# Optimization experiments

Hardware: AMD Instinct MI355X
Metric: run time of the kernel (lower is better)

Reference implementation:

```python
import jax, jax.numpy as jnp
import numpy as np

B, A = 4096, 8          # episodes, agents per episode
N = B * A               # total nodes
E = B * A * (A - 1)     # fully-connected directed edges within each group
F_IN, D, H, M, NA = 64, 64, 4, 64, 10  # in_feat, gnn_dim, heads, mem_dim, n_actions
NEG_SLOPE = 0.2
LN_EPS = 1e-5


def _build_edge_index():
    base = np.arange(A)
    s = np.repeat(base, A)
    d = np.tile(base, A)
    keep = s != d
    s, d = s[keep], d[keep]                       # [A*(A-1)]
    offs = (np.arange(B) * A)[:, None]
    src = (offs + s[None, :]).reshape(-1)
    dst = (offs + d[None, :]).reshape(-1)
    return jnp.asarray(np.stack([src, dst]), dtype=jnp.int32)  # [2, E]


def setup_inputs() -> dict:
    key = jax.random.key(0)
    ks = jax.random.split(key, 16)
    sc = 0.05
    return {
        "x": jax.random.normal(ks[0], (N, F_IN), jnp.float32),
        "edge_attr": jax.random.normal(ks[1], (E, 3), jnp.float32),
        "hidden": jax.random.normal(ks[2], (N, M), jnp.float32) * sc,
        "edge_index": _build_edge_index(),
        # GATv2 params
        "Wl": jax.random.normal(ks[3], (H * D, F_IN), jnp.float32) * sc,
        "bl": jnp.zeros((H * D,), jnp.float32),
        "Wr": jax.random.normal(ks[4], (H * D, F_IN), jnp.float32) * sc,
        "br": jnp.zeros((H * D,), jnp.float32),
        "We": jax.random.normal(ks[5], (H * D, 3), jnp.float32) * sc,
        "be": jnp.zeros((H * D,), jnp.float32),
        "att": jax.random.normal(ks[6], (H, D), jnp.float32) * sc,
        "bias_g": jnp.zeros((D,), jnp.float32),
        # GRUCell params (gate order r,z,n as in torch)
        "W_ih": jax.random.normal(ks[7], (3 * M, D), jnp.float32) * sc,
        "W_hh": jax.random.normal(ks[8], (3 * M, M), jnp.float32) * sc,
        "b_ih": jnp.zeros((3 * M,), jnp.float32),
        "b_hh": jnp.zeros((3 * M,), jnp.float32),
        # LayerNorm + output Linear
        "ln_g": jnp.ones((M,), jnp.float32),
        "ln_b": jnp.zeros((M,), jnp.float32),
        "Wq": jax.random.normal(ks[9], (NA, M), jnp.float32) * sc,
        "bq": jnp.zeros((NA,), jnp.float32),
    }


def reference(x, edge_attr, hidden, edge_index, Wl, bl, Wr, br, We, be, att,
              bias_g, W_ih, W_hh, b_ih, b_hh, ln_g, ln_b, Wq, bq):
    src, dst = edge_index[0], edge_index[1]
    # GATv2Conv (concat=False -> mean over heads), share_weights=False
    xl = (x @ Wl.T + bl).reshape(N, H, D)          # source projection
    xr = (x @ Wr.T + br).reshape(N, H, D)          # target projection
    ee = (edge_attr @ We.T + be).reshape(E, H, D)  # edge embedding
    m = jax.nn.leaky_relu(xl[src] + xr[dst] + ee, NEG_SLOPE)  # [E,H,D]
    logits = jnp.einsum('ehd,hd->eh', m, att)                  # [E,H]
    lmax = jax.ops.segment_max(logits, dst, num_segments=N)    # [N,H]
    ex = jnp.exp(logits - lmax[dst])
    denom = jax.ops.segment_sum(ex, dst, num_segments=N)       # [N,H]
    alpha = ex / denom[dst]                                    # softmax per target
    agg = jax.ops.segment_sum(alpha[:, :, None] * xl[src], dst, num_segments=N)  # [N,H,D]
    h_gnn = jax.nn.relu(agg.mean(axis=1) + bias_g)             # [N,D]
    # GRUCell
    gi = h_gnn @ W_ih.T + b_ih
    gh = hidden @ W_hh.T + b_hh
    ir, iz, inn = jnp.split(gi, 3, axis=-1)
    hr, hz, hn = jnp.split(gh, 3, axis=-1)
    r = jax.nn.sigmoid(ir + hr)
    z = jax.nn.sigmoid(iz + hz)
    n = jnp.tanh(inn + r * hn)
    h = (1.0 - z) * n + z * hidden                              # [N,M]
    # LayerNorm + Linear head
    mu = h.mean(axis=-1, keepdims=True)
    var = ((h - mu) ** 2).mean(axis=-1, keepdims=True)
    hln = (h - mu) / jnp.sqrt(var + LN_EPS) * ln_g + ln_b
    q = hln @ Wq.T + bq                                         # [N,NA]
    return q, h
```

## Files before the change

kernel.cpp:

```cpp
#include <hip/hip_runtime.h>

typedef unsigned short u16;
typedef __attribute__((ext_vector_type(8))) short bf16x8;
typedef __attribute__((ext_vector_type(4))) float f32x4;

#define NAG 8
#define FIN 64
#define MDIM 64
#define NACT 10
#define EPG 56
#define NTOT 32768
#define ABP 72
#define XLS 296
#define XHS 72

#define U_XR 2368
#define U_RZ 0
#define U_IN 1024
#define U_HN 1536
#define U_LN 2048

__device__ __forceinline__ float b2f(u16 u) {
  return __uint_as_float(((unsigned int)u) << 16);
}
__device__ __forceinline__ u16 f2b(float f) {
  unsigned int x = __float_as_uint(f);
  unsigned int r = x + 0x7fffu + ((x >> 16) & 1u);
  return (u16)(r >> 16);
}

__global__ __launch_bounds__(256) void prep_weights(
    const float* __restrict__ Wl, const float* __restrict__ Wr,
    const float* __restrict__ Wih, const float* __restrict__ Whh,
    u16* __restrict__ wsB)
{
  const int idx = blockIdx.x * 256 + threadIdx.x;
  if (idx >= 56 * 2 * 64) return;
  const int L  = idx & 63;
  const int ks = (idx >> 6) & 1;
  const int T  = idx >> 7;
  const float* W; int row0;
  if      (T < 16) { W = Wl;  row0 = T * 16; }
  else if (T < 32) { W = Wr;  row0 = (T - 16) * 16; }
  else if (T < 44) { W = Wih; row0 = (T - 32) * 16; }
  else             { W = Whh; row0 = (T - 44) * 16; }
  const int row = row0 + (L & 15);
  const int k0  = ks * 32 + (L >> 4) * 8;
  u16 v[8];
#pragma unroll
  for (int j = 0; j < 8; j++) v[j] = f2b(W[row * 64 + k0 + j]);
  *(bf16x8*)(wsB + (size_t)idx * 8) = *(bf16x8*)v;
}

__global__ __launch_bounds__(256, 4) void gnn_rnn_kernel(
    const float* __restrict__ x, const float* __restrict__ edge_attr,
    const float* __restrict__ hidden,
    const float* __restrict__ bl, const float* __restrict__ br,
    const float* __restrict__ We, const float* __restrict__ be,
    const float* __restrict__ att, const float* __restrict__ bias_g,
    const float* __restrict__ b_ih, const float* __restrict__ b_hh,
    const float* __restrict__ ln_g, const float* __restrict__ ln_b,
    const float* __restrict__ Wq, const float* __restrict__ bq,
    const u16* __restrict__ wsB,
    float* __restrict__ d_out)
{
  __shared__ __align__(16) char uraw[10368];
  __shared__ __align__(16) u16 s_xb[NAG * ABP];
  __shared__ __align__(16) u16 s_hidb[NAG * ABP];
  __shared__ __align__(16) u16 s_hgb[NAG * ABP];
  __shared__ __align__(16) float s_hid[NAG * MDIM];
  __shared__ float s_ea[EPG * 3];
  __shared__ __align__(16) u16 s_blb[256], s_brb[256];
  __shared__ __align__(16) u16 s_w0b[288], s_w1b[288], s_w2b[288], s_beb[288], s_attb[288];
  __shared__ float s_alpha[EPG][4];
  __shared__ float s_bih[192], s_bhh[192];

  u16*   uXL = (u16*)uraw;
  u16*   uXR = (u16*)uraw + U_XR;
  float* uF  = (float*)uraw;

  const int t = threadIdx.x;
  const int b = blockIdx.x;
  const int L = t & 63;
  const int w = t >> 6;
  const int q = L >> 4;

  {
    const float* xb = x + b * (NAG * FIN);
    const float* hb = hidden + b * (NAG * MDIM);
#pragma unroll
    for (int i = t; i < NAG * FIN; i += 256) {
      const int a = i >> 6, m = i & 63;
      s_xb[a * ABP + m] = f2b(xb[i]);
      const float hv = hb[i];
      s_hid[a * MDIM + m] = hv;
      s_hidb[a * ABP + m] = f2b(hv);
    }
    const float* eb = edge_attr + b * (EPG * 3);
    if (t < EPG * 3) s_ea[t] = eb[t];
    s_blb[t] = f2b(bl[t]);  s_brb[t] = f2b(br[t]);
    {
      const int h = t >> 6, d = t & 63, idx = h * XHS + d;
      s_beb[idx]  = f2b(be[t]);
      s_attb[idx] = f2b(att[t]);
      s_w0b[idx]  = f2b(We[t * 3]);
      s_w1b[idx]  = f2b(We[t * 3 + 1]);
      s_w2b[idx]  = f2b(We[t * 3 + 2]);
    }
    if (t < 192)  { s_bih[t] = b_ih[t]; s_bhh[t] = b_hh[t]; }
  }
  __syncthreads();

  {
    const int arow = L & 7;
    bf16x8 af0 = *(const bf16x8*)&s_xb[arow * ABP + q * 8];
    bf16x8 af1 = *(const bf16x8*)&s_xb[arow * ABP + 32 + q * 8];
    const bf16x8* wsBv = (const bf16x8*)wsB;
#pragma unroll 4
    for (int i = 0; i < 8; i++) {
      const int T = w * 8 + i;
      f32x4 acc = {0.f, 0.f, 0.f, 0.f};
      acc = __builtin_amdgcn_mfma_f32_16x16x32_bf16(af0, wsBv[(T * 2 + 0) * 64 + L], acc, 0, 0, 0);
      acc = __builtin_amdgcn_mfma_f32_16x16x32_bf16(af1, wsBv[(T * 2 + 1) * 64 + L], acc, 0, 0, 0);
      if (q < 2) {
        const int col = L & 15;
        const int Tm = T & 15;
        const int h = Tm >> 2, d = (Tm & 3) * 16 + col;
        const int gc = Tm * 16 + col;
        if (T < 16) {
          const float bias = b2f(s_blb[gc]);
#pragma unroll
          for (int r = 0; r < 4; r++)
            uXL[(q * 4 + r) * XLS + h * XHS + d] = f2b(acc[r] + bias);
        } else {
          const float bias = b2f(s_brb[gc]);
#pragma unroll
          for (int r = 0; r < 4; r++)
            uXR[(q * 4 + r) * XLS + h * XHS + d] = f2b(acc[r] + bias);
        }
      }
    }
  }
  __syncthreads();

  if (t < EPG * 4) {
    const int e = t % 56, h = t / 56;
    const int s = e / 7, k = e % 7;
    const int j = k + (k >= s ? 1 : 0);
    const float ea0 = s_ea[e * 3], ea1 = s_ea[e * 3 + 1], ea2 = s_ea[e * 3 + 2];
    const u16* xlp = uXL + s * XLS + h * XHS;
    const u16* xrp = uXR + j * XLS + h * XHS;
    const u16* w0p = s_w0b + h * XHS;
    const u16* w1p = s_w1b + h * XHS;
    const u16* w2p = s_w2b + h * XHS;
    const u16* bep = s_beb + h * XHS;
    const u16* atp = s_attb + h * XHS;
    float lg = 0.f;
#pragma unroll 2
    for (int kq = 0; kq < 8; kq++) {
      bf16x8 vxl = *(const bf16x8*)(xlp + kq * 8);
      bf16x8 vxr = *(const bf16x8*)(xrp + kq * 8);
      bf16x8 v0  = *(const bf16x8*)(w0p + kq * 8);
      bf16x8 v1  = *(const bf16x8*)(w1p + kq * 8);
      bf16x8 v2  = *(const bf16x8*)(w2p + kq * 8);
      bf16x8 vb  = *(const bf16x8*)(bep + kq * 8);
      bf16x8 va  = *(const bf16x8*)(atp + kq * 8);
#pragma unroll
      for (int c = 0; c < 8; c++) {
        float mv = b2f((u16)vxl[c]) + b2f((u16)vxr[c])
                 + ea0 * b2f((u16)v0[c]) + ea1 * b2f((u16)v1[c])
                 + ea2 * b2f((u16)v2[c]) + b2f((u16)vb[c]);
        mv = mv > 0.f ? mv : 0.2f * mv;
        lg += mv * b2f((u16)va[c]);
      }
    }
    s_alpha[e][h] = lg;
  }
  __syncthreads();

  if (t < 32) {
    const int j = t >> 2, h = t & 3;
    float mx = -1e30f;
#pragma unroll
    for (int s = 0; s < 8; s++) {
      if (s == j) continue;
      int e = s * 7 + (j > s ? j - 1 : j);
      mx = fmaxf(mx, s_alpha[e][h]);
    }
    float sum = 0.f;
#pragma unroll
    for (int s = 0; s < 8; s++) {
      if (s == j) continue;
      int e = s * 7 + (j > s ? j - 1 : j);
      float ex = __expf(s_alpha[e][h] - mx);
      s_alpha[e][h] = ex;
      sum += ex;
    }
    float inv = 1.f / sum;
#pragma unroll
    for (int s = 0; s < 8; s++) {
      if (s == j) continue;
      int e = s * 7 + (j > s ? j - 1 : j);
      s_alpha[e][h] *= inv;
    }
  }
  __syncthreads();

  if (t < 128) {
    const int jj = t >> 4, dq = t & 15;
    float acc[4] = {0.f, 0.f, 0.f, 0.f};
#pragma unroll 2
    for (int h = 0; h < 4; h++) {
#pragma unroll
      for (int s = 0; s < 8; s++) {
        if (s == jj) continue;
        int e = s * 7 + (jj > s ? jj - 1 : jj);
        float al = s_alpha[e][h];
        const u16* xp = uXL + s * XLS + h * XHS + dq * 4;
        ushort4 xv = *(const ushort4*)xp;
        acc[0] += al * b2f(xv.x);
        acc[1] += al * b2f(xv.y);
        acc[2] += al * b2f(xv.z);
        acc[3] += al * b2f(xv.w);
      }
    }
    const f32x4 bg = *(const f32x4*)(bias_g + dq * 4);
    u16 pk[4];
#pragma unroll
    for (int c = 0; c < 4; c++) {
      float v = acc[c] * 0.25f + bg[c];
      pk[c] = f2b(v > 0.f ? v : 0.f);
    }
    *(uint2*)&s_hgb[jj * ABP + dq * 4] = *(uint2*)pk;
  }
  __syncthreads();

  {
    const int arow = L & 7;
    bf16x8 ag0 = *(const bf16x8*)&s_hgb[arow * ABP + q * 8];
    bf16x8 ag1 = *(const bf16x8*)&s_hgb[arow * ABP + 32 + q * 8];
    bf16x8 ah0 = *(const bf16x8*)&s_hidb[arow * ABP + q * 8];
    bf16x8 ah1 = *(const bf16x8*)&s_hidb[arow * ABP + 32 + q * 8];
    const bf16x8* wsBv = (const bf16x8*)wsB;
#pragma unroll
    for (int i = 0; i < 3; i++) {
      const int T6 = w * 3 + i;
      const int Tg = 32 + T6, Th = 44 + T6;
      f32x4 acci = {0.f, 0.f, 0.f, 0.f};
      acci = __builtin_amdgcn_mfma_f32_16x16x32_bf16(ag0, wsBv[(Tg * 2 + 0) * 64 + L], acci, 0, 0, 0);
      acci = __builtin_amdgcn_mfma_f32_16x16x32_bf16(ag1, wsBv[(Tg * 2 + 1) * 64 + L], acci, 0, 0, 0);
      f32x4 acch = {0.f, 0.f, 0.f, 0.f};
      acch = __builtin_amdgcn_mfma_f32_16x16x32_bf16(ah0, wsBv[(Th * 2 + 0) * 64 + L], acch, 0, 0, 0);
      acch = __builtin_amdgcn_mfma_f32_16x16x32_bf16(ah1, wsBv[(Th * 2 + 1) * 64 + L], acch, 0, 0, 0);
      if (q < 2) {
        const int col = L & 15;
        const int gc = T6 * 16 + col;
        if (T6 < 8) {
#pragma unroll
          for (int r = 0; r < 4; r++)
            uF[U_RZ + (q * 4 + r) * 128 + gc] = acci[r] + acch[r] + s_bih[gc] + s_bhh[gc];
        } else {
#pragma unroll
          for (int r = 0; r < 4; r++) {
            uF[U_IN + (q * 4 + r) * 64 + gc - 128] = acci[r] + s_bih[gc];
            uF[U_HN + (q * 4 + r) * 64 + gc - 128] = acch[r] + s_bhh[gc];
          }
        }
      }
    }
  }
  __syncthreads();

  {
    const float lng = ln_g[L];
    const float lnb = ln_b[L];
#pragma unroll
    for (int rr = 0; rr < 2; rr++) {
      const int a = w + rr * 4, m = L;
      float rz_r = uF[U_RZ + a * 128 + m];
      float rz_z = uF[U_RZ + a * 128 + 64 + m];
      float inn  = uF[U_IN + a * 64 + m];
      float hn   = uF[U_HN + a * 64 + m];
      float r = 1.f / (1.f + __expf(-rz_r));
      float z = 1.f / (1.f + __expf(-rz_z));
      float xg = inn + r * hn;
      xg = fminf(fmaxf(xg, -20.f), 20.f);
      float e2 = __expf(2.f * xg);
      float n = (e2 - 1.f) / (e2 + 1.f);
      float hv = (1.f - z) * n + z * s_hid[a * MDIM + m];
      d_out[NTOT * NACT + (b * NAG + a) * MDIM + m] = hv;
      float sum = hv;
#pragma unroll
      for (int off = 1; off < 64; off <<= 1) sum += __shfl_xor(sum, off, 64);
      float mu = sum * (1.f / 64.f);
      float dv = hv - mu;
      float s2 = dv * dv;
#pragma unroll
      for (int off = 1; off < 64; off <<= 1) s2 += __shfl_xor(s2, off, 64);
      float var = s2 * (1.f / 64.f);
      uF[U_LN + a * 68 + m] = dv * rsqrtf(var + 1e-5f) * lng + lnb;
    }
  }
  __syncthreads();

  if (t < NAG * NACT) {
    const int a = t / NACT, o = t % NACT;
    float acc = bq[o];
    const float4* lv = (const float4*)(uF + U_LN + a * 68);
    const float4* wv = (const float4*)(Wq + o * 64);
#pragma unroll 4
    for (int kq = 0; kq < 16; kq++) {
      float4 l4 = lv[kq], w4 = wv[kq];
      acc += l4.x * w4.x + l4.y * w4.y + l4.z * w4.z + l4.w * w4.w;
    }
    d_out[(b * NAG + a) * NACT + o] = acc;
  }
}

extern "C" void kernel_launch(void* const* d_in, const int* in_sizes, int n_in,
                              void* d_out, int out_size, void* d_ws, size_t ws_size,
                              hipStream_t stream) {
  const int N  = in_sizes[0] / FIN;
  const int Bn = N / NAG;
  u16* wsB = (u16*)d_ws;

  prep_weights<<<28, 256, 0, stream>>>(
      (const float*)d_in[4],
      (const float*)d_in[6],
      (const float*)d_in[12],
      (const float*)d_in[13],
      wsB);

  gnn_rnn_kernel<<<Bn, 256, 0, stream>>>(
      (const float*)d_in[0], (const float*)d_in[1], (const float*)d_in[2],
      (const float*)d_in[5],
      (const float*)d_in[7],
      (const float*)d_in[8],
      (const float*)d_in[9],
      (const float*)d_in[10],
      (const float*)d_in[11],
      (const float*)d_in[14],
      (const float*)d_in[15],
      (const float*)d_in[16], (const float*)d_in[17],
      (const float*)d_in[18], (const float*)d_in[19],
      wsB, (float*)d_out);
}
```

Before: 161.4 us.

## Process two episodes per block to fill MFMA rows and halve block count

```diff
diff --git a/kernel.cpp b/kernel.cpp
--- a/kernel.cpp
+++ b/kernel.cpp
@@ -5,6 +5,7 @@
 typedef __attribute__((ext_vector_type(4))) float f32x4;
 
 #define NAG 8
+#define NAGB 16
 #define FIN 64
 #define MDIM 64
 #define NACT 10
@@ -14,11 +15,11 @@
 #define XLS 296
 #define XHS 72
 
-#define U_XR 2368
+#define U_XR 4736
 #define U_RZ 0
-#define U_IN 1024
-#define U_HN 1536
-#define U_LN 2048
+#define U_IN 2048
+#define U_HN 3072
+#define U_LN 4096
 
 __device__ __forceinline__ float b2f(u16 u) {
   return __uint_as_float(((unsigned int)u) << 16);
@@ -64,15 +65,14 @@
     const u16* __restrict__ wsB,
     float* __restrict__ d_out)
 {
-  __shared__ __align__(16) char uraw[10368];
-  __shared__ __align__(16) u16 s_xb[NAG * ABP];
-  __shared__ __align__(16) u16 s_hidb[NAG * ABP];
-  __shared__ __align__(16) u16 s_hgb[NAG * ABP];
-  __shared__ __align__(16) float s_hid[NAG * MDIM];
-  __shared__ float s_ea[EPG * 3];
+  __shared__ __align__(16) char uraw[20736];
+  __shared__ __align__(16) u16 s_xb[NAGB * ABP];
+  __shared__ __align__(16) u16 s_hidb[NAGB * ABP];
+  __shared__ __align__(16) u16 s_hgb[NAGB * ABP];
+  __shared__ float s_ea[2 * EPG * 3];
   __shared__ __align__(16) u16 s_blb[256], s_brb[256];
   __shared__ __align__(16) u16 s_w0b[288], s_w1b[288], s_w2b[288], s_beb[288], s_attb[288];
-  __shared__ float s_alpha[EPG][4];
+  __shared__ float s_alpha[2 * EPG][4];
   __shared__ float s_bih[192], s_bhh[192];
 
   u16*   uXL = (u16*)uraw;
@@ -86,18 +86,16 @@
   const int q = L >> 4;
 
   {
-    const float* xb = x + b * (NAG * FIN);
-    const float* hb = hidden + b * (NAG * MDIM);
-#pragma unroll
-    for (int i = t; i < NAG * FIN; i += 256) {
+    const float* xb = x + b * (NAGB * FIN);
+    const float* hb = hidden + b * (NAGB * MDIM);
+#pragma unroll
+    for (int i = t; i < NAGB * FIN; i += 256) {
       const int a = i >> 6, m = i & 63;
       s_xb[a * ABP + m] = f2b(xb[i]);
-      const float hv = hb[i];
-      s_hid[a * MDIM + m] = hv;
-      s_hidb[a * ABP + m] = f2b(hv);
-    }
-    const float* eb = edge_attr + b * (EPG * 3);
-    if (t < EPG * 3) s_ea[t] = eb[t];
+      s_hidb[a * ABP + m] = f2b(hb[i]);
+    }
+    const float* eb = edge_attr + b * (2 * EPG * 3);
+    for (int i = t; i < 2 * EPG * 3; i += 256) s_ea[i] = eb[i];
     s_blb[t] = f2b(bl[t]);  s_brb[t] = f2b(br[t]);
     {
       const int h = t >> 6, d = t & 63, idx = h * XHS + d;
@@ -112,7 +110,7 @@
   __syncthreads();
 
   {
-    const int arow = L & 7;
+    const int arow = L & 15;
     bf16x8 af0 = *(const bf16x8*)&s_xb[arow * ABP + q * 8];
     bf16x8 af1 = *(const bf16x8*)&s_xb[arow * ABP + 32 + q * 8];
     const bf16x8* wsBv = (const bf16x8*)wsB;
@@ -122,76 +120,78 @@
       f32x4 acc = {0.f, 0.f, 0.f, 0.f};
       acc = __builtin_amdgcn_mfma_f32_16x16x32_bf16(af0, wsBv[(T * 2 + 0) * 64 + L], acc, 0, 0, 0);
       acc = __builtin_amdgcn_mfma_f32_16x16x32_bf16(af1, wsBv[(T * 2 + 1) * 64 + L], acc, 0, 0, 0);
-      if (q < 2) {
-        const int col = L & 15;
-        const int Tm = T & 15;
-        const int h = Tm >> 2, d = (Tm & 3) * 16 + col;
-        const int gc = Tm * 16 + col;
-        if (T < 16) {
-          const float bias = b2f(s_blb[gc]);
-#pragma unroll
-          for (int r = 0; r < 4; r++)
-            uXL[(q * 4 + r) * XLS + h * XHS + d] = f2b(acc[r] + bias);
-        } else {
-          const float bias = b2f(s_brb[gc]);
-#pragma unroll
-          for (int r = 0; r < 4; r++)
-            uXR[(q * 4 + r) * XLS + h * XHS + d] = f2b(acc[r] + bias);
+      const int col = L & 15;
+      const int Tm = T & 15;
+      const int h = Tm >> 2, d = (Tm & 3) * 16 + col;
+      const int gc = Tm * 16 + col;
+      if (T < 16) {
+        const float bias = b2f(s_blb[gc]);
+#pragma unroll
+        for (int r = 0; r < 4; r++)
+          uXL[(q * 4 + r) * XLS + h * XHS + d] = f2b(acc[r] + bias);
+      } else {
+        const float bias = b2f(s_brb[gc]);
+#pragma unroll
+        for (int r = 0; r < 4; r++)
+          uXR[(q * 4 + r) * XLS + h * XHS + d] = f2b(acc[r] + bias);
+      }
+    }
+  }
+  __syncthreads();
+
+  for (int ep = 0; ep < 2; ep++) {
+    if (t < EPG * 4) {
+      const int e = t % 56, h = t / 56;
+      const int s = e / 7, k = e % 7;
+      const int j = k + (k >= s ? 1 : 0);
+      const int eg = ep * EPG + e;
+      const float ea0 = s_ea[eg * 3], ea1 = s_ea[eg * 3 + 1], ea2 = s_ea[eg * 3 + 2];
+      const u16* xlp = uXL + (ep * 8 + s) * XLS + h * XHS;
+      const u16* xrp = uXR + (ep * 8 + j) * XLS + h * XHS;
+      const u16* w0p = s_w0b + h * XHS;
+      const u16* w1p = s_w1b + h * XHS;
+      const u16* w2p = s_w2b + h * XHS;
+      const u16* bep = s_beb + h * XHS;
+      const u16* atp = s_attb + h * XHS;
+      float lg = 0.f;
+#pragma unroll 2
+      for (int kq = 0; kq < 8; kq++) {
+        bf16x8 vxl = *(const bf16x8*)(xlp + kq * 8);
+        bf16x8 vxr = *(const bf16x8*)(xrp + kq * 8);
+        bf16x8 v0  = *(const bf16x8*)(w0p + kq * 8);
+        bf16x8 v1  = *(const bf16x8*)(w1p + kq * 8);
+        bf16x8 v2  = *(const bf16x8*)(w2p + kq * 8);
+        bf16x8 vb  = *(const bf16x8*)(bep + kq * 8);
+        bf16x8 va  = *(const bf16x8*)(atp + kq * 8);
+#pragma unroll
+        for (int c = 0; c < 8; c++) {
+          float mv = b2f((u16)vxl[c]) + b2f((u16)vxr[c])
+                   + ea0 * b2f((u16)v0[c]) + ea1 * b2f((u16)v1[c])
+                   + ea2 * b2f((u16)v2[c]) + b2f((u16)vb[c]);
+          mv = mv > 0.f ? mv : 0.2f * mv;
+          lg += mv * b2f((u16)va[c]);
         }
       }
-    }
-  }
-  __syncthreads();
-
-  if (t < EPG * 4) {
-    const int e = t % 56, h = t / 56;
-    const int s = e / 7, k = e % 7;
-    const int j = k + (k >= s ? 1 : 0);
-    const float ea0 = s_ea[e * 3], ea1 = s_ea[e * 3 + 1], ea2 = s_ea[e * 3 + 2];
-    const u16* xlp = uXL + s * XLS + h * XHS;
-    const u16* xrp = uXR + j * XLS + h * XHS;
-    const u16* w0p = s_w0b + h * XHS;
-    const u16* w1p = s_w1b + h * XHS;
-    const u16* w2p = s_w2b + h * XHS;
-    const u16* bep = s_beb + h * XHS;
-    const u16* atp = s_attb + h * XHS;
-    float lg = 0.f;
-#pragma unroll 2
-    for (int kq = 0; kq < 8; kq++) {
-      bf16x8 vxl = *(const bf16x8*)(xlp + kq * 8);
-      bf16x8 vxr = *(const bf16x8*)(xrp + kq * 8);
-      bf16x8 v0  = *(const bf16x8*)(w0p + kq * 8);
-      bf16x8 v1  = *(const bf16x8*)(w1p + kq * 8);
-      bf16x8 v2  = *(const bf16x8*)(w2p + kq * 8);
-      bf16x8 vb  = *(const bf16x8*)(bep + kq * 8);
-      bf16x8 va  = *(const bf16x8*)(atp + kq * 8);
-#pragma unroll
-      for (int c = 0; c < 8; c++) {
-        float mv = b2f((u16)vxl[c]) + b2f((u16)vxr[c])
-                 + ea0 * b2f((u16)v0[c]) + ea1 * b2f((u16)v1[c])
-                 + ea2 * b2f((u16)v2[c]) + b2f((u16)vb[c]);
-        mv = mv > 0.f ? mv : 0.2f * mv;
-        lg += mv * b2f((u16)va[c]);
-      }
-    }
-    s_alpha[e][h] = lg;
-  }
-  __syncthreads();
-
-  if (t < 32) {
-    const int j = t >> 2, h = t & 3;
+      s_alpha[eg][h] = lg;
+    }
+  }
+  __syncthreads();
+
+  if (t < 64) {
+    const int ep = t >> 5, j = (t >> 2) & 7, h = t & 3;
+    const int e0 = ep * EPG;
     float mx = -1e30f;
 #pragma unroll
     for (int s = 0; s < 8; s++) {
       if (s == j) continue;
-      int e = s * 7 + (j > s ? j - 1 : j);
+      int e = e0 + s * 7 + (j > s ? j - 1 : j);
       mx = fmaxf(mx, s_alpha[e][h]);
     }
     float sum = 0.f;
 #pragma unroll
     for (int s = 0; s < 8; s++) {
       if (s == j) continue;
-      int e = s * 7 + (j > s ? j - 1 : j);
+      int e = e0 + s * 7 + (j > s ? j - 1 : j);
       float ex = __expf(s_alpha[e][h] - mx);
       s_alpha[e][h] = ex;
       sum += ex;
@@ -200,23 +200,24 @@
 #pragma unroll
     for (int s = 0; s < 8; s++) {
       if (s == j) continue;
-      int e = s * 7 + (j > s ? j - 1 : j);
+      int e = e0 + s * 7 + (j > s ? j - 1 : j);
       s_alpha[e][h] *= inv;
     }
   }
   __syncthreads();
 
-  if (t < 128) {
-    const int jj = t >> 4, dq = t & 15;
+  {
+    const int ep = t >> 7, jj = (t >> 4) & 7, dq = t & 15;
+    const int a16 = ep * 8 + jj;
     float acc[4] = {0.f, 0.f, 0.f, 0.f};
 #pragma unroll 2
     for (int h = 0; h < 4; h++) {
 #pragma unroll
       for (int s = 0; s < 8; s++) {
         if (s == jj) continue;
-        int e = s * 7 + (jj > s ? jj - 1 : jj);
+        int e = ep * EPG + s * 7 + (jj > s ? jj - 1 : jj);
         float al = s_alpha[e][h];
-        const u16* xp = uXL + s * XLS + h * XHS + dq * 4;
+        const u16* xp = uXL + (ep * 8 + s) * XLS + h * XHS + dq * 4;
         ushort4 xv = *(const ushort4*)xp;
         acc[0] += al * b2f(xv.x);
         acc[1] += al * b2f(xv.y);
@@ -231,12 +232,12 @@
       float v = acc[c] * 0.25f + bg[c];
       pk[c] = f2b(v > 0.f ? v : 0.f);
     }
-    *(uint2*)&s_hgb[jj * ABP + dq * 4] = *(uint2*)pk;
-  }
-  __syncthreads();
-
-  {
-    const int arow = L & 7;
+    *(uint2*)&s_hgb[a16 * ABP + dq * 4] = *(uint2*)pk;
+  }
+  __syncthreads();
+
+  {
+    const int arow = L & 15;
     bf16x8 ag0 = *(const bf16x8*)&s_hgb[arow * ABP + q * 8];
     bf16x8 ag1 = *(const bf16x8*)&s_hgb[arow * ABP + 32 + q * 8];
     bf16x8 ah0 = *(const bf16x8*)&s_hidb[arow * ABP + q * 8];
@@ -252,19 +253,17 @@
       f32x4 acch = {0.f, 0.f, 0.f, 0.f};
       acch = __builtin_amdgcn_mfma_f32_16x16x32_bf16(ah0, wsBv[(Th * 2 + 0) * 64 + L], acch, 0, 0, 0);
       acch = __builtin_amdgcn_mfma_f32_16x16x32_bf16(ah1, wsBv[(Th * 2 + 1) * 64 + L], acch, 0, 0, 0);
-      if (q < 2) {
-        const int col = L & 15;
-        const int gc = T6 * 16 + col;
-        if (T6 < 8) {
-#pragma unroll
-          for (int r = 0; r < 4; r++)
-            uF[U_RZ + (q * 4 + r) * 128 + gc] = acci[r] + acch[r] + s_bih[gc] + s_bhh[gc];
-        } else {
-#pragma unroll
-          for (int r = 0; r < 4; r++) {
-            uF[U_IN + (q * 4 + r) * 64 + gc - 128] = acci[r] + s_bih[gc];
-            uF[U_HN + (q * 4 + r) * 64 + gc - 128] = acch[r] + s_bhh[gc];
-          }
+      const int col = L & 15;
+      const int gc = T6 * 16 + col;
+      if (T6 < 8) {
+#pragma unroll
+        for (int r = 0; r < 4; r++)
+          uF[U_RZ + (q * 4 + r) * 128 + gc] = acci[r] + acch[r] + s_bih[gc] + s_bhh[gc];
+      } else {
+#pragma unroll
+        for (int r = 0; r < 4; r++) {
+          uF[U_IN + (q * 4 + r) * 64 + gc - 128] = acci[r] + s_bih[gc];
+          uF[U_HN + (q * 4 + r) * 64 + gc - 128] = acch[r] + s_bhh[gc];
         }
       }
     }
@@ -275,20 +274,21 @@
     const float lng = ln_g[L];
     const float lnb = ln_b[L];
 #pragma unroll
-    for (int rr = 0; rr < 2; rr++) {
+    for (int rr = 0; rr < 4; rr++) {
       const int a = w + rr * 4, m = L;
       float rz_r = uF[U_RZ + a * 128 + m];
       float rz_z = uF[U_RZ + a * 128 + 64 + m];
       float inn  = uF[U_IN + a * 64 + m];
       float hn   = uF[U_HN + a * 64 + m];
+      float hid  = hidden[(b * NAGB + a) * MDIM + m];
       float r = 1.f / (1.f + __expf(-rz_r));
       float z = 1.f / (1.f + __expf(-rz_z));
       float xg = inn + r * hn;
       xg = fminf(fmaxf(xg, -20.f), 20.f);
       float e2 = __expf(2.f * xg);
       float n = (e2 - 1.f) / (e2 + 1.f);
-      float hv = (1.f - z) * n + z * s_hid[a * MDIM + m];
-      d_out[NTOT * NACT + (b * NAG + a) * MDIM + m] = hv;
+      float hv = (1.f - z) * n + z * hid;
+      d_out[NTOT * NACT + (b * NAGB + a) * MDIM + m] = hv;
       float sum = hv;
 #pragma unroll
       for (int off = 1; off < 64; off <<= 1) sum += __shfl_xor(sum, off, 64);
@@ -303,7 +303,7 @@
   }
   __syncthreads();
 
-  if (t < NAG * NACT) {
+  if (t < NAGB * NACT) {
     const int a = t / NACT, o = t % NACT;
     float acc = bq[o];
     const float4* lv = (const float4*)(uF + U_LN + a * 68);
@@ -313,7 +313,7 @@
       float4 l4 = lv[kq], w4 = wv[kq];
       acc += l4.x * w4.x + l4.y * w4.y + l4.z * w4.z + l4.w * w4.w;
     }
-    d_out[(b * NAG + a) * NACT + o] = acc;
+    d_out[(b * NAGB + a) * NACT + o] = acc;
   }
 }
 
@@ -321,7 +321,7 @@
                               void* d_out, int out_size, void* d_ws, size_t ws_size,
                               hipStream_t stream) {
   const int N  = in_sizes[0] / FIN;
-  const int Bn = N / NAG;
+  const int Bn = N / NAGB;
   u16* wsB = (u16*)d_ws;
 
   prep_weights<<<28, 256, 0, stream>>>(
```

New measurement: 157.3 us. 2.6% less time.
